# Kernel tuning notes

Measured on AMD Instinct MI355X. Metric: run time of the kernel, lower is better.

The kernel has to match this reference:

```python
import jax, jax.numpy as jnp
import numpy as np

N = 8192        # particles
NBH = 64        # black holes
L = 46.0        # box side -> ~32 neighbors per particle at radius 4.5
K = 4           # kernel_size per axis
KK = K * K * K
EXTENT = 9.0    # radius_scale(1.5) * 6 * particle_radius(1)
EXTENT_BH = 4.0 * EXTENT
EP = 300000     # padded particle-particle edge count
EB = 160000     # padded bh->particle edge count
CIN = 4         # vel(3) + mass(1)
C0, C1, C2, C3 = 32, 64, 64, 3
FOUR_OVER_PI = 4.0 / np.pi


def _ball_query_np(query, points, radius, cap, pad_seg):
    """Brute-force host-side ball query. Returns padded (src, dst); padding
    uses dst == pad_seg (a sentinel segment that is dropped later)."""
    r2 = radius * radius
    src, dst = [], []
    for i in range(0, query.shape[0], 1024):
        q = query[i:i + 1024]
        d2 = ((q[:, None, :] - points[None, :, :]) ** 2).sum(-1)
        m = (d2 < r2) & (d2 > 0.0)  # radius_search_ignore_query_points
        qi, pj = np.nonzero(m)
        dst.append(qi + i)
        src.append(pj)
    src = np.concatenate(src).astype(np.int32)
    dst = np.concatenate(dst).astype(np.int32)
    n = min(len(src), cap)
    out_s = np.zeros(cap, np.int32)
    out_d = np.full(cap, pad_seg, np.int32)
    out_s[:n] = src[:n]
    out_d[:n] = dst[:n]
    return out_s, out_d


def setup_inputs() -> dict:
    rng = np.random.RandomState(0)
    pos = (rng.rand(N, 3) * L).astype(np.float32)
    vel = rng.randn(N, 3).astype(np.float32)
    mass = rng.rand(N).astype(np.float32)
    bh_pos = (rng.rand(NBH, 3) * L).astype(np.float32)
    bh_vel = rng.randn(NBH, 3).astype(np.float32)
    bh_mass = (rng.rand(NBH) * 10.0).astype(np.float32)
    pp_src, pp_dst = _ball_query_np(pos, pos, EXTENT * 0.5, EP, N)
    bh_src, bh_dst = _ball_query_np(pos, bh_pos, EXTENT_BH * 0.5, EB, N)

    def w(*s):
        return (rng.randn(*s) * 0.05).astype(np.float32)

    inp = dict(
        pos=jnp.asarray(pos), vel=jnp.asarray(vel), mass=jnp.asarray(mass),
        bh_pos=jnp.asarray(bh_pos), bh_vel=jnp.asarray(bh_vel), bh_mass=jnp.asarray(bh_mass),
        pp_src=jnp.asarray(pp_src), pp_dst=jnp.asarray(pp_dst),
        bh_src=jnp.asarray(bh_src), bh_dst=jnp.asarray(bh_dst),
        W0a=jnp.asarray(w(K, K, K, CIN, C0)), b0a=jnp.zeros(C0, jnp.float32),
        Wd0=jnp.asarray(w(CIN, C0)), bd0=jnp.zeros(C0, jnp.float32),
        W0b=jnp.asarray(w(K, K, K, CIN, C0)), b0b=jnp.zeros(C0, jnp.float32),
        W1=jnp.asarray(w(K, K, K, 3 * C0, C1)), b1=jnp.zeros(C1, jnp.float32),
        Wd1=jnp.asarray(w(3 * C0, C1)), bd1=jnp.zeros(C1, jnp.float32),
        W2=jnp.asarray(w(K, K, K, C1, C2)), b2=jnp.zeros(C2, jnp.float32),
        Wd2=jnp.asarray(w(C1, C2)), bd2=jnp.zeros(C2, jnp.float32),
        W3=jnp.asarray(w(K, K, K, C2, C3)), b3=jnp.zeros(C3, jnp.float32),
        Wd3=jnp.asarray(w(C2, C3)), bd3=jnp.zeros(C3, jnp.float32),
    )
    return inp


def _ball_to_cube(p):
    """Volume-preserving map from unit ball to cube [-1,1]^3 (sphere->cylinder->cube)."""
    eps = 1e-8
    x, y, z = p[..., 0], p[..., 1], p[..., 2]
    sq = x * x + y * y + z * z
    nrm = jnp.sqrt(sq)
    xy = x * x + y * y
    # sphere -> cylinder
    caps = 1.25 * z * z > xy
    s_caps = jnp.sqrt(3.0 * nrm / (nrm + jnp.abs(z) + eps))
    s_side = nrm / jnp.sqrt(xy + eps)
    s = jnp.where(caps, s_caps, s_side)
    valid = sq > eps
    cx = jnp.where(valid, x * s, 0.0)
    cy = jnp.where(valid, y * s, 0.0)
    cz = jnp.where(valid, jnp.where(caps, jnp.sign(z) * nrm, 1.5 * z), 0.0)
    # cylinder -> cube (concentric disc-to-square, area preserving)
    rxy = jnp.sqrt(cx * cx + cy * cy)
    regA = cx * cx >= cy * cy
    safe_cx = jnp.where(jnp.abs(cx) > eps, cx, 1.0)
    safe_cy = jnp.where(jnp.abs(cy) > eps, cy, 1.0)
    uA = jnp.sign(cx) * rxy
    vA = uA * FOUR_OVER_PI * jnp.arctan(cy / safe_cx)
    vB = jnp.sign(cy) * rxy
    uB = vB * FOUR_OVER_PI * jnp.arctan(cx / safe_cy)
    okxy = rxy > eps
    u = jnp.where(okxy, jnp.where(regA, uA, uB), 0.0)
    v = jnp.where(okxy, jnp.where(regA, vA, vB), 0.0)
    return jnp.stack([u, v, cz], axis=-1)


def _cconv(feats, pos_src, pos_dst, src, dst, W, b, extent):
    """ContinuousConv: ball-query edges (src->dst), poly6 window, trilinear
    kernel interpolation (align_corners=True), scatter-sum, no normalization."""
    n_out = pos_dst.shape[0]
    radius = 0.5 * extent
    ps = jnp.take(pos_src, src, axis=0)                       # [E,3]
    pd = jnp.take(pos_dst, jnp.minimum(dst, n_out - 1), axis=0)
    d = (ps - pd) * (1.0 / radius)                            # normalized offsets
    r_sqr = jnp.sum(d * d, axis=-1)
    win = jnp.clip((1.0 - r_sqr) ** 3, 0.0, 1.0)              # window_poly6
    u = _ball_to_cube(d)                                      # in [-1,1]^3
    t = (u + 1.0) * (0.5 * (K - 1))                           # align_corners grid coords
    i0f = jnp.clip(jnp.floor(t), 0, K - 2)
    i0 = i0f.astype(jnp.int32)
    f = t - i0f                                               # trilinear fractions
    fe = jnp.take(feats, src, axis=0) * win[:, None]          # [E,Cin]
    Cin = feats.shape[1]
    Wf = W.reshape(KK, Cin, -1)
    T = jnp.zeros(((n_out + 1) * KK, Cin), feats.dtype)
    for dx in (0, 1):
        wx = f[:, 0] if dx else 1.0 - f[:, 0]
        for dy in (0, 1):
            wy = f[:, 1] if dy else 1.0 - f[:, 1]
            for dz in (0, 1):
                wz = f[:, 2] if dz else 1.0 - f[:, 2]
                k = ((i0[:, 0] + dx) * K + (i0[:, 1] + dy)) * K + (i0[:, 2] + dz)
                idx = dst * KK + k                            # sentinel dst==n_out dropped
                T = T + jax.ops.segment_sum((wx * wy * wz)[:, None] * fe, idx,
                                            num_segments=(n_out + 1) * KK)
    T = T.reshape(n_out + 1, KK, Cin)[:n_out]                 # [N,64,Cin]
    return jnp.einsum('nkc,kcd->nd', T, Wf) + b


def _forward(pos, vel, mass, bh_pos, bh_vel, bh_mass,
             W0a, b0a, Wd0, bd0, W0b, b0b, W1, b1, Wd1, bd1,
             W2, b2, Wd2, bd2, W3, b3, Wd3, bd3,
             pp_src, pp_dst, bh_src, bh_dst):
    feats = jnp.concatenate([vel, mass[:, None]], axis=-1)        # [N,4]
    bh_feats = jnp.concatenate([bh_vel, bh_mass[:, None]], axis=-1)
    c0 = _cconv(feats, pos, pos, pp_src, pp_dst, W0a, b0a, EXTENT)      # [N,32]
    d0 = feats @ Wd0 + bd0                                               # [N,32]
    cb = _cconv(bh_feats, bh_pos, pos, bh_src, bh_dst, W0b, b0b, EXTENT_BH)
    h = jnp.concatenate([c0, cb, d0], axis=-1)                           # [N,96]
    c1 = jax.nn.relu(_cconv(h, pos, pos, pp_src, pp_dst, W1, b1, EXTENT))
    d1 = jax.nn.relu(h @ Wd1 + bd1)
    h1 = c1 + d1                                                         # 64 != 96 -> no residual
    c2 = jax.nn.relu(_cconv(h1, pos, pos, pp_src, pp_dst, W2, b2, EXTENT))
    d2 = jax.nn.relu(h1 @ Wd2 + bd2)
    h2 = c2 + d2 + h1                                                    # 64 == 64 -> residual
    c3 = _cconv(h2, pos, pos, pp_src, pp_dst, W3, b3, EXTENT)
    d3 = h2 @ Wd3 + bd3
    return c3 + d3                                                       # accelerations [N,3]


def reference(pos, vel, mass, bh_pos, bh_vel, bh_mass,
              pp_src, pp_dst, bh_src, bh_dst,
              W0a, b0a, Wd0, bd0, W0b, b0b, W1, b1, Wd1, bd1,
              W2, b2, Wd2, bd2, W3, b3, Wd3, bd3):
    return _forward(pos, vel, mass, bh_pos, bh_vel, bh_mass,
                    W0a, b0a, Wd0, bd0, W0b, b0b, W1, b1, Wd1, bd1,
                    W2, b2, Wd2, bd2, W3, b3, Wd3, bd3,
                    pp_src, pp_dst, bh_src, bh_dst)
```

## Files before the change

kernel.cpp:

```cpp
#include <hip/hip_runtime.h>
#include <math.h>

#define NPART 8192
#define NBHX  64
#define EPX   300000
#define EBX   160000
#define FOUR_OVER_PI 1.27323954473516f

typedef __attribute__((ext_vector_type(8))) short bf16x8;
typedef __attribute__((ext_vector_type(4))) float f32x4;

__device__ __forceinline__ float signf(float x){ return (x>0.f)?1.f:((x<0.f)?-1.f:0.f); }
__device__ __forceinline__ unsigned short f2bf(float f){
  unsigned u = __float_as_uint(f);
  u += 0x7FFFu + ((u >> 16) & 1u);
  return (unsigned short)(u >> 16);
}
__device__ __forceinline__ float bf2f(unsigned short h){
  return __uint_as_float(((unsigned)h) << 16);
}
__device__ __forceinline__ float bfl(unsigned u){ return __uint_as_float(u << 16); }
__device__ __forceinline__ float bfh(unsigned u){ return __uint_as_float(u & 0xffff0000u); }

__global__ void geom2_kernel(const float* __restrict__ pos, const float* __restrict__ bh_pos,
                             const int* __restrict__ srcP, const int* __restrict__ dstP,
                             const int* __restrict__ srcB, const int* __restrict__ dstB,
                             uint2* __restrict__ gewP, uint2* __restrict__ gewB,
                             int* __restrict__ hist) {
  int idx = blockIdx.x*256 + threadIdx.x;
  if (idx < 4096) hist[idx] = 0;
  bool isP = idx < EPX;
  int e = isP ? idx : idx - EPX;
  if (!isP && e >= EBX) return;
  const int* src = isP ? srcP : srcB;
  const int* dst = isP ? dstP : dstB;
  const float* ppos = isP ? pos : bh_pos;
  uint2* gew = isP ? gewP : gewB;
  float inv_radius = isP ? (1.f/4.5f) : (1.f/18.f);
  int s = src[e], t = dst[e];
  if (t >= NPART) {
    uint2 z; z.x = s*64; z.y = 0;
    for (int j=0;j<8;j++) gew[(size_t)e*8+j] = z;
    return;
  }
  float x = (ppos[s*3+0] - pos[t*3+0]) * inv_radius;
  float y = (ppos[s*3+1] - pos[t*3+1]) * inv_radius;
  float z = (ppos[s*3+2] - pos[t*3+2]) * inv_radius;
  float r2 = x*x + y*y + z*z;
  float w1 = 1.f - r2;
  float win = fminf(fmaxf(w1*w1*w1, 0.f), 1.f);
  const float eps = 1e-8f;
  float nrm = sqrtf(r2);
  float xy = x*x + y*y;
  bool caps = (1.25f*z*z > xy);
  float s_caps = sqrtf(3.f*nrm/(nrm + fabsf(z) + eps));
  float s_side = nrm / sqrtf(xy + eps);
  float sc = caps ? s_caps : s_side;
  bool valid = r2 > eps;
  float cx = valid ? x*sc : 0.f;
  float cy = valid ? y*sc : 0.f;
  float cz = valid ? (caps ? signf(z)*nrm : 1.5f*z) : 0.f;
  float rxy = sqrtf(cx*cx + cy*cy);
  bool regA = (cx*cx >= cy*cy);
  float safe_cx = (fabsf(cx) > eps) ? cx : 1.0f;
  float safe_cy = (fabsf(cy) > eps) ? cy : 1.0f;
  float uA = signf(cx)*rxy;
  float vA = uA * FOUR_OVER_PI * atanf(cy/safe_cx);
  float vB = signf(cy)*rxy;
  float uB = vB * FOUR_OVER_PI * atanf(cx/safe_cy);
  bool okxy = rxy > eps;
  float u = okxy ? (regA ? uA : uB) : 0.f;
  float v = okxy ? (regA ? vA : vB) : 0.f;
  float tt[3] = { (u+1.f)*1.5f, (v+1.f)*1.5f, (cz+1.f)*1.5f };
  int i0[3]; float f[3];
#pragma unroll
  for (int ax=0; ax<3; ax++) {
    float tf = floorf(tt[ax]);
    tf = fminf(fmaxf(tf, 0.f), 2.f);
    i0[ax] = (int)tf;
    f[ax] = tt[ax] - tf;
  }
  unsigned sb = s*64 + ((i0[0]*4 + i0[1])*4 + i0[2]);
#pragma unroll
  for (int j=0;j<8;j++) {
    float wx = (j&4) ? f[0] : 1.f - f[0];
    float wy = (j&2) ? f[1] : 1.f - f[1];
    float wz = (j&1) ? f[2] : 1.f - f[2];
    uint2 o; o.x = sb; o.y = __float_as_uint(win * wx * wy * wz);
    gew[(size_t)e*8+j] = o;
  }
}

__global__ void prep_kernel(const float* __restrict__ vel, const float* __restrict__ mass,
                            const float* __restrict__ bhvel, const float* __restrict__ bhmass,
                            float* __restrict__ feats, float* __restrict__ bhfeats,
                            const int* __restrict__ dstP, const int* __restrict__ dstB,
                            int* __restrict__ rsP, int* __restrict__ rsB) {
  int i = blockIdx.x*256 + threadIdx.x;
  if (i < NPART) {
    feats[i*4+0]=vel[i*3+0]; feats[i*4+1]=vel[i*3+1]; feats[i*4+2]=vel[i*3+2]; feats[i*4+3]=mass[i];
  }
  if (i < NBHX) {
    bhfeats[i*4+0]=bhvel[i*3+0]; bhfeats[i*4+1]=bhvel[i*3+1]; bhfeats[i*4+2]=bhvel[i*3+2]; bhfeats[i*4+3]=bhmass[i];
  }
  if (i <= NPART) {
    int lo = 0, hi = EPX;
    while (lo < hi) { int mid = (lo+hi)>>1; if (dstP[mid] < i) lo = mid+1; else hi = mid; }
    rsP[i] = lo;
  }
  int k = i - (NPART+1);
  if (k >= 0 && k <= NPART) {
    int lo = 0, hi = EBX;
    while (lo < hi) { int mid = (lo+hi)>>1; if (dstB[mid] < k) lo = mid+1; else hi = mid; }
    rsB[k] = lo;
  }
}

__global__ void cellw_kernel(const float* __restrict__ pos, int* __restrict__ cell,
                             int* __restrict__ hist,
                             const float* __restrict__ W1, const float* __restrict__ W2,
                             const float* __restrict__ W3,
                             unsigned short* __restrict__ BT1, unsigned short* __restrict__ BT2,
                             unsigned short* __restrict__ BT3) {
  int b = blockIdx.x;
  if (b < 32) {
    int i = b*256 + threadIdx.x;
    const float inv = 16.0f/46.0f;
    int ix = min(15, max(0, (int)(pos[i*3+0]*inv)));
    int iy = min(15, max(0, (int)(pos[i*3+1]*inv)));
    int iz = min(15, max(0, (int)(pos[i*3+2]*inv)));
    int c = (ix*16+iy)*16+iz;
    cell[i] = c;
    atomicAdd(&hist[c], 1);
    return;
  }
  int idx = (b-32)*256 + threadIdx.x;
  const int S1 = 4096*96, S2 = 4096*64, S3 = 256*64;
  if (idx < S1) {
    int n = idx/96, c = idx - n*96; int k = n>>6, d = n&63;
    BT1[idx] = f2bf(W1[((size_t)k*96 + c)*64 + d]);
  } else if (idx < S1+S2) {
    int t = idx - S1; int n = t>>6, c = t&63; int k = n>>6, d = n&63;
    BT2[t] = f2bf(W2[((size_t)k*64 + c)*64 + d]);
  } else if (idx < S1+S2+S3) {
    int t = idx - S1 - S2; int n = t>>6, c = t&63; int k = n>>2, d = n&3;
    BT3[t] = f2bf((d < 3) ? W3[((size_t)k*64 + c)*3 + d] : 0.f);
  }
}

__global__ __launch_bounds__(256) void scan_kernel(const int* __restrict__ hist, int* __restrict__ offs) {
  __shared__ int wsum[4];
  int t = threadIdx.x;
  int base = t*16;
  int loc[16]; int s = 0;
#pragma unroll
  for (int i=0;i<16;i++){ loc[i]=s; s+=hist[base+i]; }
  int lane = t & 63, wv = t >> 6;
  int pre = s;
  for (int off=1; off<64; off<<=1) {
    int v = __shfl_up(pre, off);
    if (lane >= off) pre += v;
  }
  if (lane == 63) wsum[wv] = pre;
  __syncthreads();
  int wbase = 0;
  for (int w=0; w<wv; w++) wbase += wsum[w];
  int ex = wbase + pre - s;
#pragma unroll
  for (int i=0;i<16;i++) offs[base+i] = ex + loc[i];
}
__global__ void scatterorder_kernel(const int* __restrict__ cell, int* __restrict__ offs,
                                    int* __restrict__ order) {
  int i = blockIdx.x*256 + threadIdx.x;
  if (i >= NPART) return;
  int p = atomicAdd(&offs[cell[i]], 1);
  order[p] = i;
}

__device__ __forceinline__ int swz_block(int bid, int nb) {
  return (bid & 7)*(nb >> 3) + (bid >> 3);
}

__global__ void y0_kernel(const float* __restrict__ feats4, const float* __restrict__ bhfeats,
                          const float* __restrict__ W0a, const float* __restrict__ W0b,
                          unsigned short* __restrict__ Y0a, unsigned short* __restrict__ Y0b) {
  int idx = blockIdx.x*256 + threadIdx.x;
  if (idx >= (NPART+NBHX)*256) return;
  int oct = idx & 3, k = (idx>>2) & 63, s = idx >> 8;
  bool bh = (s >= NPART);
  int sl = bh ? s - NPART : s;
  const float* fp = (bh ? bhfeats : feats4) + (size_t)sl*4;
  const float* W0 = bh ? W0b : W0a;
  unsigned short* Y = (bh ? Y0b : Y0a) + ((size_t)sl*64 + k)*32 + oct*8;
  float4 f = *(const float4*)fp;
  const float* w = W0 + (size_t)k*128 + oct*8;
  unsigned short o[8];
#pragma unroll
  for (int i=0;i<8;i++) {
    float v = f.x*w[i] + f.y*w[32+i] + f.z*w[64+i] + f.w*w[96+i];
    o[i] = f2bf(v);
  }
  uint4 u;
  u.x = (unsigned)o[0] | ((unsigned)o[1]<<16);
  u.y = (unsigned)o[2] | ((unsigned)o[3]<<16);
  u.z = (unsigned)o[4] | ((unsigned)o[5]<<16);
  u.w = (unsigned)o[6] | ((unsigned)o[7]<<16);
  *(uint4*)Y = u;
}

__global__ __launch_bounds__(256) void gemm_y_kernel(
    const unsigned short* __restrict__ A, const unsigned short* __restrict__ BT,
    int KC, int Ntot, unsigned short* __restrict__ Y) {
  const int wid  = threadIdx.x >> 6;
  const int lane = threadIdx.x & 63;
// ... 16 lines not shown
      bf16x8 b = *(const bf16x8*)(BT + (size_t)(n0 + n*16 + r)*KC + ko);
      acc[0][n] = __builtin_amdgcn_mfma_f32_16x16x32_bf16(a0, b, acc[0][n], 0, 0, 0);
      acc[1][n] = __builtin_amdgcn_mfma_f32_16x16x32_bf16(a1, b, acc[1][n], 0, 0, 0);
    }
  }
#pragma unroll
  for (int h=0;h<2;h++)
#pragma unroll
    for (int n=0;n<4;n++)
#pragma unroll
      for (int j=0;j<4;j++)
        Y[(size_t)(m0 + h*16 + g*4 + j)*Ntot + n0 + n*16 + r] = f2bf(acc[h][n][j]);
}

__device__ __forceinline__ void xor_add4(f32x4& a, int mask) {
  a.x += __shfl_xor(a.x, mask);
  a.y += __shfl_xor(a.y, mask);
  a.z += __shfl_xor(a.z, mask);
  a.w += __shfl_xor(a.w, mask);
}

__global__ __launch_bounds__(256) void gather_l0_kernel(
    const int* __restrict__ order,
    const int* __restrict__ rsP, const uint2* __restrict__ gewP,
    const int* __restrict__ rsB, const uint2* __restrict__ gewB,
    const unsigned short* __restrict__ Y0a, const unsigned short* __restrict__ Y0b,
    const float* __restrict__ feats4, const float* __restrict__ Wd0, const float* __restrict__ bd0,
    const float* __restrict__ b0a, const float* __restrict__ b0b,
    float* __restrict__ hf, unsigned short* __restrict__ hb) {
  const int sw = swz_block(blockIdx.x, gridDim.x);
  const int node = order[sw*4 + (threadIdx.x >> 6)];
  const int lane = threadIdx.x & 63;
  const int j = lane >> 3, cg = lane & 7;
  const int koff = ((j&4)<<2) | ((j&2)<<1) | (j&1);
  f32x4 accP = {0.f,0.f,0.f,0.f}, accB = {0.f,0.f,0.f,0.f};
  {
    int e0 = rsP[node], e1 = rsP[node+1];
    int e = e0;
    for (; e + 4 <= e1; e += 4) {
      uint2 p[4]; uint2 y[4];
#pragma unroll
      for (int i=0;i<4;i++) p[i] = gewP[(size_t)(e+i)*8 + j];
#pragma unroll
      for (int i=0;i<4;i++) y[i] = *(const uint2*)(Y0a + ((size_t)(p[i].x + koff))*32 + cg*4);
#pragma unroll
      for (int i=0;i<4;i++) {
        float w = __uint_as_float(p[i].y);
        accP.x += w*bfl(y[i].x); accP.y += w*bfh(y[i].x);
        accP.z += w*bfl(y[i].y); accP.w += w*bfh(y[i].y);
      }
    }
    for (; e < e1; e++) {
      uint2 p = gewP[(size_t)e*8 + j];
      uint2 y = *(const uint2*)(Y0a + ((size_t)(p.x + koff))*32 + cg*4);
      float w = __uint_as_float(p.y);
      accP.x += w*bfl(y.x); accP.y += w*bfh(y.x);
      accP.z += w*bfl(y.y); accP.w += w*bfh(y.y);
    }
  }
  {
    int e0 = rsB[node], e1 = rsB[node+1];
    int e = e0;
    for (; e + 4 <= e1; e += 4) {
      uint2 p[4]; uint2 y[4];
#pragma unroll
      for (int i=0;i<4;i++) p[i] = gewB[(size_t)(e+i)*8 + j];
#pragma unroll
      for (int i=0;i<4;i++) y[i] = *(const uint2*)(Y0b + ((size_t)(p[i].x + koff))*32 + cg*4);
#pragma unroll
      for (int i=0;i<4;i++) {
        float w = __uint_as_float(p[i].y);
        accB.x += w*bfl(y[i].x); accB.y += w*bfh(y[i].x);
        accB.z += w*bfl(y[i].y); accB.w += w*bfh(y[i].y);
      }
    }
    for (; e < e1; e++) {
      uint2 p = gewB[(size_t)e*8 + j];
      uint2 y = *(const uint2*)(Y0b + ((size_t)(p.x + koff))*32 + cg*4);
      float w = __uint_as_float(p.y);
      accB.x += w*bfl(y.x); accB.y += w*bfh(y.x);
      accB.z += w*bfl(y.y); accB.w += w*bfh(y.y);
    }
  }
  xor_add4(accP, 8);  xor_add4(accP, 16); xor_add4(accP, 32);
  xor_add4(accB, 8);  xor_add4(accB, 16); xor_add4(accB, 32);
  if (lane < 8) {
    float4 f = *(const float4*)(feats4 + (size_t)node*4);
    float4 ba = *(const float4*)(b0a + cg*4);
    float4 bb = *(const float4*)(b0b + cg*4);
    float4 bdv = *(const float4*)(bd0 + cg*4);
    float4 w0v = *(const float4*)(Wd0 + 0*32 + cg*4);
    float4 w1v = *(const float4*)(Wd0 + 1*32 + cg*4);
    float4 w2v = *(const float4*)(Wd0 + 2*32 + cg*4);
    float4 w3v = *(const float4*)(Wd0 + 3*32 + cg*4);
    float4 dd;
    dd.x = bdv.x + f.x*w0v.x + f.y*w1v.x + f.z*w2v.x + f.w*w3v.x;
    dd.y = bdv.y + f.x*w0v.y + f.y*w1v.y + f.z*w2v.y + f.w*w3v.y;
    dd.z = bdv.z + f.x*w0v.z + f.y*w1v.z + f.z*w2v.z + f.w*w3v.z;
    dd.w = bdv.w + f.x*w0v.w + f.y*w1v.w + f.z*w2v.w + f.w*w3v.w;
    float4 c0; c0.x = accP.x + ba.x; c0.y = accP.y + ba.y; c0.z = accP.z + ba.z; c0.w = accP.w + ba.w;
    float4 cb; cb.x = accB.x + bb.x; cb.y = accB.y + bb.y; cb.z = accB.z + bb.z; cb.w = accB.w + bb.w;
    size_t o = (size_t)node*96;
    *(float4*)(hf + o + cg*4)      = c0;
    *(float4*)(hf + o + 32 + cg*4) = cb;
    *(float4*)(hf + o + 64 + cg*4) = dd;
    ushort4 u0 = {f2bf(c0.x), f2bf(c0.y), f2bf(c0.z), f2bf(c0.w)};
    ushort4 u1 = {f2bf(cb.x), f2bf(cb.y), f2bf(cb.z), f2bf(cb.w)};
    ushort4 u2 = {f2bf(dd.x), f2bf(dd.y), f2bf(dd.z), f2bf(dd.w)};
    *(ushort4*)(hb + o + cg*4)      = u0;
    *(ushort4*)(hb + o + 32 + cg*4) = u1;
    *(ushort4*)(hb + o + 64 + cg*4) = u2;
  }
}

template<int DCIN, bool ADDSKIP>
__global__ __launch_bounds__(128) void gather64_kernel(
    const int* __restrict__ order,
    const int* __restrict__ rs, const uint2* __restrict__ gew,
    const unsigned short* __restrict__ Y,
    const float* __restrict__ Xf, const float* __restrict__ Wd, const float* __restrict__ bd,
    const float* __restrict__ bconv, const float* __restrict__ skip,
    float* __restrict__ outf, unsigned short* __restrict__ outb) {
  const int sw = swz_block(blockIdx.x, gridDim.x);
  const int node = order[sw];
  const int wave = threadIdx.x >> 6;
  const int lane = threadIdx.x & 63;
  const int j = lane >> 3, cg = lane & 7;
  const int koff = ((j&4)<<2) | ((j&2)<<1) | (j&1);
  __shared__ __align__(16) float red[64*16];
  f32x4 accA = {0.f,0.f,0.f,0.f}, accB = {0.f,0.f,0.f,0.f};
  const int e0 = rs[node], e1 = rs[node+1];
  int e = e0 + wave;
  for (; e + 6 < e1; e += 8) {
    uint2 p[4]; uint4 y[4];
#pragma unroll
    for (int i=0;i<4;i++) p[i] = gew[(size_t)(e + i*2)*8 + j];
#pragma unroll
    for (int i=0;i<4;i++) y[i] = *(const uint4*)(Y + ((size_t)(p[i].x + koff))*64 + cg*8);
#pragma unroll
    for (int i=0;i<4;i++) {
      float w = __uint_as_float(p[i].y);
      accA.x += w*bfl(y[i].x); accA.y += w*bfh(y[i].x);
      accA.z += w*bfl(y[i].y); accA.w += w*bfh(y[i].y);
      accB.x += w*bfl(y[i].z); accB.y += w*bfh(y[i].z);
      accB.z += w*bfl(y[i].w); accB.w += w*bfh(y[i].w);
    }
  }
  for (; e < e1; e += 2) {
    uint2 p = gew[(size_t)e*8 + j];
    uint4 y = *(const uint4*)(Y + ((size_t)(p.x + koff))*64 + cg*8);
    float w = __uint_as_float(p.y);
    accA.x += w*bfl(y.x); accA.y += w*bfh(y.x);
    accA.z += w*bfl(y.y); accA.w += w*bfh(y.y);
    accB.x += w*bfl(y.z); accB.y += w*bfh(y.z);
    accB.z += w*bfl(y.w); accB.w += w*bfh(y.w);
  }
  constexpr int KQ = DCIN/16;
  f32x4 ddA = {0.f,0.f,0.f,0.f}, ddB = {0.f,0.f,0.f,0.f};
  {
    const int seg = wave*8 + j;
    const float* x = Xf + (size_t)node*DCIN + seg*KQ;
#pragma unroll
    for (int kk=0; kk<KQ; kk++) {
      float xv = x[kk];
      float4 w0 = *(const float4*)(Wd + (size_t)(seg*KQ+kk)*64 + cg*8);
      float4 w1 = *(const float4*)(Wd + (size_t)(seg*KQ+kk)*64 + cg*8 + 4);
      ddA.x += xv*w0.x; ddA.y += xv*w0.y; ddA.z += xv*w0.z; ddA.w += xv*w0.w;
      ddB.x += xv*w1.x; ddB.y += xv*w1.y; ddB.z += xv*w1.z; ddB.w += xv*w1.w;
    }
  }
  if (wave == 1) {
    *(f32x4*)(red + lane*16)      = accA;
    *(f32x4*)(red + lane*16 + 4)  = accB;
    *(f32x4*)(red + lane*16 + 8)  = ddA;
    *(f32x4*)(red + lane*16 + 12) = ddB;
  }
  __syncthreads();
  if (wave == 0) {
    {
      f32x4 oA = *(const f32x4*)(red + lane*16);
      f32x4 oB = *(const f32x4*)(red + lane*16 + 4);
      f32x4 oC = *(const f32x4*)(red + lane*16 + 8);
      f32x4 oD = *(const f32x4*)(red + lane*16 + 12);
      accA.x += oA.x; accA.y += oA.y; accA.z += oA.z; accA.w += oA.w;
      accB.x += oB.x; accB.y += oB.y; accB.z += oB.z; accB.w += oB.w;
      ddA.x += oC.x; ddA.y += oC.y; ddA.z += oC.z; ddA.w += oC.w;
      ddB.x += oD.x; ddB.y += oD.y; ddB.z += oD.z; ddB.w += oD.w;
    }
    xor_add4(accA, 8); xor_add4(accA, 16); xor_add4(accA, 32);
    xor_add4(accB, 8); xor_add4(accB, 16); xor_add4(accB, 32);
    xor_add4(ddA, 8);  xor_add4(ddA, 16);  xor_add4(ddA, 32);
    xor_add4(ddB, 8);  xor_add4(ddB, 16);  xor_add4(ddB, 32);
    if (lane < 8) {
      float4 bc0 = *(const float4*)(bconv + cg*8);
      float4 bc1 = *(const float4*)(bconv + cg*8 + 4);
      float4 bd0v = *(const float4*)(bd + cg*8);
      float4 bd1v = *(const float4*)(bd + cg*8 + 4);
      float4 v0, v1;
      v0.x = fmaxf(accA.x + bc0.x, 0.f) + fmaxf(ddA.x + bd0v.x, 0.f);
      v0.y = fmaxf(accA.y + bc0.y, 0.f) + fmaxf(ddA.y + bd0v.y, 0.f);
      v0.z = fmaxf(accA.z + bc0.z, 0.f) + fmaxf(ddA.z + bd0v.z, 0.f);
      v0.w = fmaxf(accA.w + bc0.w, 0.f) + fmaxf(ddA.w + bd0v.w, 0.f);
      v1.x = fmaxf(accB.x + bc1.x, 0.f) + fmaxf(ddB.x + bd1v.x, 0.f);
      v1.y = fmaxf(accB.y + bc1.y, 0.f) + fmaxf(ddB.y + bd1v.y, 0.f);
      v1.z = fmaxf(accB.z + bc1.z, 0.f) + fmaxf(ddB.z + bd1v.z, 0.f);
      v1.w = fmaxf(accB.w + bc1.w, 0.f) + fmaxf(ddB.w + bd1v.w, 0.f);
      if (ADDSKIP) {
        float4 s0 = *(const float4*)(skip + (size_t)node*64 + cg*8);
        float4 s1 = *(const float4*)(skip + (size_t)node*64 + cg*8 + 4);
        v0.x += s0.x; v0.y += s0.y; v0.z += s0.z; v0.w += s0.w;
        v1.x += s1.x; v1.y += s1.y; v1.z += s1.z; v1.w += s1.w;
      }
      *(float4*)(outf + (size_t)node*64 + cg*8)     = v0;
      *(float4*)(outf + (size_t)node*64 + cg*8 + 4) = v1;
      ushort4 u0 = {f2bf(v0.x), f2bf(v0.y), f2bf(v0.z), f2bf(v0.w)};
      ushort4 u1 = {f2bf(v1.x), f2bf(v1.y), f2bf(v1.z), f2bf(v1.w)};
      *(ushort4*)(outb + (size_t)node*64 + cg*8)     = u0;
      *(ushort4*)(outb + (size_t)node*64 + cg*8 + 4) = u1;
    }
  }
}

__global__ __launch_bounds__(256) void gather3_kernel(
    const int* __restrict__ order,
    const int* __restrict__ rs, const uint2* __restrict__ gew,
    const unsigned short* __restrict__ Y3,
    const float* __restrict__ h2f, const float* __restrict__ Wd3, const float* __restrict__ bd3,
    const float* __restrict__ b3, float* __restrict__ out) {
  const int sw = swz_block(blockIdx.x, gridDim.x);
  const int node = order[sw*4 + (threadIdx.x >> 6)];
  const int lane = threadIdx.x & 63;
  const int e2 = lane >> 5, j = (lane >> 2) & 7, dd = lane & 3;
  const int koff = ((j&4)<<2)|((j&2)<<1)|(j&1);
  float acc = 0.f;
  const int e0 = rs[node], e1 = rs[node+1];
  for (int e = e0; e < e1; e += 2) {
    int ee = e + e2;
    bool v = ee < e1;
    int ix = v ? ee : e;
    uint2 p = gew[(size_t)ix*8 + j];
    float w = v ? __uint_as_float(p.y) : 0.f;
    acc += w * bf2f(Y3[((size_t)(p.x + koff))*4 + dd]);
  }
  acc += __shfl_xor(acc, 4);
  acc += __shfl_xor(acc, 8);
  acc += __shfl_xor(acc, 16);
  acc += __shfl_down(acc, 32);
  if (lane < 3) {
    float d3 = bd3[lane];
    const float* x = h2f + (size_t)node*64;
#pragma unroll 8
    for (int c=0;c<64;c++) d3 += x[c]*Wd3[c*3 + lane];
    out[(size_t)node*3 + lane] = acc + b3[lane] + d3;
  }
}

extern "C" void kernel_launch(void* const* d_in, const int* in_sizes, int n_in,
                              void* d_out, int out_size, void* d_ws, size_t ws_size,
                              hipStream_t stream) {
  const float* pos    = (const float*)d_in[0];
  const float* vel    = (const float*)d_in[1];
  const float* mass   = (const float*)d_in[2];
  const float* bh_pos = (const float*)d_in[3];
  const float* bh_vel = (const float*)d_in[4];
  const float* bh_mass= (const float*)d_in[5];
  const int* pp_src   = (const int*)d_in[6];
  const int* pp_dst   = (const int*)d_in[7];
  const int* bh_src   = (const int*)d_in[8];
  const int* bh_dst   = (const int*)d_in[9];
  const float* W0a=(const float*)d_in[10]; const float* b0a=(const float*)d_in[11];
  const float* Wd0=(const float*)d_in[12]; const float* bd0=(const float*)d_in[13];
  const float* W0b=(const float*)d_in[14]; const float* b0b=(const float*)d_in[15];
  const float* W1 =(const float*)d_in[16]; const float* b1 =(const float*)d_in[17];
  const float* Wd1=(const float*)d_in[18]; const float* bd1=(const float*)d_in[19];
  const float* W2 =(const float*)d_in[20]; const float* b2 =(const float*)d_in[21];
  const float* Wd2=(const float*)d_in[22]; const float* bd2=(const float*)d_in[23];
  const float* W3 =(const float*)d_in[24]; const float* b3 =(const float*)d_in[25];
  const float* Wd3=(const float*)d_in[26]; const float* bd3=(const float*)d_in[27];
  float* out = (float*)d_out;
  char* wsb = (char*)d_ws;

  size_t off = 0;
  auto alloc = [&](size_t nbytes){ size_t o = off; off += (nbytes + 255) & ~((size_t)255); return o; };
  size_t feats_o   = alloc((size_t)NPART*4*4);
  size_t bhfeats_o = alloc((size_t)NBHX*4*4);
  size_t rs_pp_o   = alloc(8256*4);
  size_t rs_bh_o   = alloc(8256*4);
  size_t gew_pp_o  = alloc((size_t)EPX*8*8);
  size_t gew_bh_o  = alloc((size_t)EBX*8*8);
  size_t hf_o  = alloc((size_t)NPART*96*4);
  size_t hb_o  = alloc((size_t)NPART*96*2);
  size_t h1f_o = alloc((size_t)NPART*64*4);
  size_t h1b_o = alloc((size_t)NPART*64*2);
  size_t h2f_o = alloc((size_t)NPART*64*4);
  size_t h2b_o = alloc((size_t)NPART*64*2);
  size_t bt1_o = alloc((size_t)4096*96*2);
  size_t bt2_o = alloc((size_t)4096*64*2);
  size_t bt3_o = alloc((size_t)256*64*2);
  size_t y0b_o = alloc((size_t)NBHX*64*32*2);
  size_t cell_o = alloc((size_t)NPART*4);
  size_t hist_o = alloc((size_t)4096*4);
  size_t order_o= alloc((size_t)NPART*4);
  size_t y_o   = alloc((size_t)NPART*4096*2);

  float* featsP = (float*)(wsb + feats_o); float* bhfeatsP = (float*)(wsb + bhfeats_o);
  int* rsPP = (int*)(wsb + rs_pp_o); int* rsBH = (int*)(wsb + rs_bh_o);
  uint2* gewP = (uint2*)(wsb + gew_pp_o);
  uint2* gewB = (uint2*)(wsb + gew_bh_o);
  float* hf  = (float*)(wsb + hf_o);  unsigned short* hb  = (unsigned short*)(wsb + hb_o);
  float* h1f = (float*)(wsb + h1f_o); unsigned short* h1b = (unsigned short*)(wsb + h1b_o);
  float* h2f = (float*)(wsb + h2f_o); unsigned short* h2b = (unsigned short*)(wsb + h2b_o);
  unsigned short* BT1 = (unsigned short*)(wsb + bt1_o);
  unsigned short* BT2 = (unsigned short*)(wsb + bt2_o);
  unsigned short* BT3 = (unsigned short*)(wsb + bt3_o);
  unsigned short* Y0b = (unsigned short*)(wsb + y0b_o);
  int* cellA = (int*)(wsb + cell_o);
  int* histA = (int*)(wsb + hist_o);
  int* orderA= (int*)(wsb + order_o);
  unsigned short* Ybuf = (unsigned short*)(wsb + y_o);

  geom2_kernel<<<(EPX+EBX+255)/256, 256, 0, stream>>>(pos, bh_pos, pp_src, pp_dst, bh_src, bh_dst,
                                                      gewP, gewB, histA);
  prep_kernel<<<(2*(NPART+1)+255)/256, 256, 0, stream>>>(vel, mass, bh_vel, bh_mass,
                                                         featsP, bhfeatsP, pp_dst, bh_dst, rsPP, rsBH);
  cellw_kernel<<<32 + (4096*96 + 4096*64 + 256*64 + 255)/256, 256, 0, stream>>>(
      pos, cellA, histA, W1, W2, W3, BT1, BT2, BT3);
  scan_kernel<<<1, 256, 0, stream>>>(histA, histA);
  scatterorder_kernel<<<NPART/256, 256, 0, stream>>>(cellA, histA, orderA);

  y0_kernel<<<((NPART+NBHX)*256+255)/256, 256, 0, stream>>>(featsP, bhfeatsP, W0a, W0b, Ybuf, Y0b);
  gather_l0_kernel<<<NPART/4, 256, 0, stream>>>(orderA, rsPP, gewP, rsBH, gewB,
                                                Ybuf, Y0b, featsP, Wd0, bd0, b0a, b0b, hf, hb);
  {
    dim3 g(NPART/128, 4096/64);
    gemm_y_kernel<<<g, 256, 0, stream>>>(hb, BT1, 96, 4096, Ybuf);
    gather64_kernel<96,false><<<NPART, 128, 0, stream>>>(orderA, rsPP, gewP, Ybuf,
        hf, Wd1, bd1, b1, nullptr, h1f, h1b);
  }
  {
    dim3 g(NPART/128, 4096/64);
    gemm_y_kernel<<<g, 256, 0, stream>>>(h1b, BT2, 64, 4096, Ybuf);
    gather64_kernel<64,true><<<NPART, 128, 0, stream>>>(orderA, rsPP, gewP, Ybuf,
        h1f, Wd2, bd2, b2, h1f, h2f, h2b);
  }
  {
    dim3 g(NPART/128, 256/64);
    gemm_y_kernel<<<g, 256, 0, stream>>>(h2b, BT3, 64, 256, Ybuf);
    gather3_kernel<<<NPART/4, 256, 0, stream>>>(orderA, rsPP, gewP, Ybuf,
        h2f, Wd3, bd3, b3, out);
  }
}
```

Before: 219.6 us.

## Compress edge records to one 16-byte entry and store features in spatial order

Each edge used to be written as 8 corner entries of index plus weight. It is now a single 16-byte record: a base index, fp16 fractional coordinates and two z-weights pre-multiplied by the window. The gather kernels rebuild each corner weight on the fly, which cuts edge-table traffic in every layer pass. Intermediate features (Y, hf, h1, h2) are now stored in the spatially sorted order through an inverse permutation, so gathered rows are more likely to be local in cache. The costs are a few extra multiplies per gathered corner, fp16 rounding of the fractions, and a reordering of kernel launches so geometry runs after the sort.

```diff
diff --git a/kernel.cpp b/kernel.cpp
--- a/kernel.cpp
+++ b/kernel.cpp
@@ -21,26 +21,135 @@
 }
 __device__ __forceinline__ float bfl(unsigned u){ return __uint_as_float(u << 16); }
 __device__ __forceinline__ float bfh(unsigned u){ return __uint_as_float(u & 0xffff0000u); }
+__device__ __forceinline__ float f16tof(unsigned short h){
+  _Float16 v = __builtin_bit_cast(_Float16, h);
+  return (float)v;
+}
+__device__ __forceinline__ unsigned short ftof16(float f){
+  _Float16 v = (_Float16)f;
+  return __builtin_bit_cast(unsigned short, v);
+}
+__device__ __forceinline__ float corner_w(const uint4& r, int j){
+  float fx = f16tof((unsigned short)(r.y & 0xffffu));
+  float fy = f16tof((unsigned short)(r.y >> 16));
+  float wx = (j&4) ? fx : 1.f - fx;
+  float wy = (j&2) ? fy : 1.f - fy;
+  float wz = __uint_as_float((j&1) ? r.w : r.z);
+  return wx*wy*wz;
+}
+
+__global__ void prep_kernel(const float* __restrict__ vel, const float* __restrict__ mass,
+                            const float* __restrict__ bhvel, const float* __restrict__ bhmass,
+                            float* __restrict__ feats, float* __restrict__ bhfeats,
+                            const int* __restrict__ dstP, const int* __restrict__ dstB,
+                            int* __restrict__ rsP, int* __restrict__ rsB,
+                            int* __restrict__ hist) {
+  int i = blockIdx.x*256 + threadIdx.x;
+  if (i < 4096) hist[i] = 0;
+  if (i < NPART) {
+    feats[i*4+0]=vel[i*3+0]; feats[i*4+1]=vel[i*3+1]; feats[i*4+2]=vel[i*3+2]; feats[i*4+3]=mass[i];
+  }
+  if (i < NBHX) {
+    bhfeats[i*4+0]=bhvel[i*3+0]; bhfeats[i*4+1]=bhvel[i*3+1]; bhfeats[i*4+2]=bhvel[i*3+2]; bhfeats[i*4+3]=bhmass[i];
+  }
+  if (i <= NPART) {
+    int lo = 0, hi = EPX;
+    while (lo < hi) { int mid = (lo+hi)>>1; if (dstP[mid] < i) lo = mid+1; else hi = mid; }
+    rsP[i] = lo;
+  }
+  int k = i - (NPART+1);
+  if (k >= 0 && k <= NPART) {
+    int lo = 0, hi = EBX;
+    while (lo < hi) { int mid = (lo+hi)>>1; if (dstB[mid] < k) lo = mid+1; else hi = mid; }
+    rsB[k] = lo;
+  }
+}
+
+__global__ void cellw_kernel(const float* __restrict__ pos, int* __restrict__ cell,
+                             int* __restrict__ hist,
+                             const float* __restrict__ W1, const float* __restrict__ W2,
+                             const float* __restrict__ W3,
+                             unsigned short* __restrict__ BT1, unsigned short* __restrict__ BT2,
+                             unsigned short* __restrict__ BT3) {
+  int b = blockIdx.x;
+  if (b < 32) {
+    int i = b*256 + threadIdx.x;
+    const float inv = 16.0f/46.0f;
+    int ix = min(15, max(0, (int)(pos[i*3+0]*inv)));
+    int iy = min(15, max(0, (int)(pos[i*3+1]*inv)));
+    int iz = min(15, max(0, (int)(pos[i*3+2]*inv)));
+    int c = (ix*16+iy)*16+iz;
+    cell[i] = c;
+    atomicAdd(&hist[c], 1);
+    return;
+  }
+  int idx = (b-32)*256 + threadIdx.x;
+  const int S1 = 4096*96, S2 = 4096*64, S3 = 256*64;
+  if (idx < S1) {
+    int n = idx/96, c = idx - n*96; int k = n>>6, d = n&63;
+    BT1[idx] = f2bf(W1[((size_t)k*96 + c)*64 + d]);
+  } else if (idx < S1+S2) {
+    int t = idx - S1; int n = t>>6, c = t&63; int k = n>>6, d = n&63;
+    BT2[t] = f2bf(W2[((size_t)k*64 + c)*64 + d]);
+  } else if (idx < S1+S2+S3) {
+    int t = idx - S1 - S2; int n = t>>6, c = t&63; int k = n>>2, d = n&3;
+    BT3[t] = f2bf((d < 3) ? W3[((size_t)k*64 + c)*3 + d] : 0.f);
+  }
+}
+
+__global__ __launch_bounds__(256) void scan_kernel(const int* __restrict__ hist, int* __restrict__ offs) {
+  __shared__ int wsum[4];
+  int t = threadIdx.x;
+  int base = t*16;
+  int loc[16]; int s = 0;
+#pragma unroll
+  for (int i=0;i<16;i++){ loc[i]=s; s+=hist[base+i]; }
+  int lane = t & 63, wv = t >> 6;
+  int pre = s;
+  for (int off=1; off<64; off<<=1) {
+    int v = __shfl_up(pre, off);
+    if (lane >= off) pre += v;
+  }
+  if (lane == 63) wsum[wv] = pre;
+  __syncthreads();
+  int wbase = 0;
+  for (int w=0; w<wv; w++) wbase += wsum[w];
+  int ex = wbase + pre - s;
+#pragma unroll
+  for (int i=0;i<16;i++) offs[base+i] = ex + loc[i];
+}
+__global__ void scatterorder_kernel(const int* __restrict__ cell, int* __restrict__ offs,
+                                    int* __restrict__ order, int* __restrict__ invp) {
+  int i = blockIdx.x*256 + threadIdx.x;
+  if (i >= NPART) return;
+  int p = atomicAdd(&offs[cell[i]], 1);
+  order[p] = i;
+  invp[i] = p;
+}
+
+__device__ __forceinline__ int swz_block(int bid, int nb) {
+  return (bid & 7)*(nb >> 3) + (bid >> 3);
+}
 
 __global__ void geom2_kernel(const float* __restrict__ pos, const float* __restrict__ bh_pos,
                              const int* __restrict__ srcP, const int* __restrict__ dstP,
                              const int* __restrict__ srcB, const int* __restrict__ dstB,
-                             uint2* __restrict__ gewP, uint2* __restrict__ gewB,
-                             int* __restrict__ hist) {
+                             const int* __restrict__ invp,
+                             uint4* __restrict__ recP, uint4* __restrict__ recB) {
   int idx = blockIdx.x*256 + threadIdx.x;
-  if (idx < 4096) hist[idx] = 0;
   bool isP = idx < EPX;
   int e = isP ? idx : idx - EPX;
   if (!isP && e >= EBX) return;
   const int* src = isP ? srcP : srcB;
   const int* dst = isP ? dstP : dstB;
   const float* ppos = isP ? pos : bh_pos;
-  uint2* gew = isP ? gewP : gewB;
+  uint4* rec = isP ? recP : recB;
   float inv_radius = isP ? (1.f/4.5f) : (1.f/18.f);
   int s = src[e], t = dst[e];
+  unsigned srow = isP ? (unsigned)invp[s] : (unsigned)s;
   if (t >= NPART) {
-    uint2 z; z.x = s*64; z.y = 0;
-    for (int j=0;j<8;j++) gew[(size_t)e*8+j] = z;
+    uint4 z; z.x = srow*64; z.y = 0; z.z = 0; z.w = 0;
+    rec[e] = z;
     return;
   }
   float x = (ppos[s*3+0] - pos[t*3+0]) * inv_radius;
@@ -80,108 +189,16 @@
     i0[ax] = (int)tf;
     f[ax] = tt[ax] - tf;
   }
-  unsigned sb = s*64 + ((i0[0]*4 + i0[1])*4 + i0[2]);
-#pragma unroll
-  for (int j=0;j<8;j++) {
-    float wx = (j&4) ? f[0] : 1.f - f[0];
-    float wy = (j&2) ? f[1] : 1.f - f[1];
-    float wz = (j&1) ? f[2] : 1.f - f[2];
-    uint2 o; o.x = sb; o.y = __float_as_uint(win * wx * wy * wz);
-    gew[(size_t)e*8+j] = o;
-  }
-}
-
-__global__ void prep_kernel(const float* __restrict__ vel, const float* __restrict__ mass,
-                            const float* __restrict__ bhvel, const float* __restrict__ bhmass,
-                            float* __restrict__ feats, float* __restrict__ bhfeats,
-                            const int* __restrict__ dstP, const int* __restrict__ dstB,
-                            int* __restrict__ rsP, int* __restrict__ rsB) {
-  int i = blockIdx.x*256 + threadIdx.x;
-  if (i < NPART) {
-    feats[i*4+0]=vel[i*3+0]; feats[i*4+1]=vel[i*3+1]; feats[i*4+2]=vel[i*3+2]; feats[i*4+3]=mass[i];
-  }
-  if (i < NBHX) {
-    bhfeats[i*4+0]=bhvel[i*3+0]; bhfeats[i*4+1]=bhvel[i*3+1]; bhfeats[i*4+2]=bhvel[i*3+2]; bhfeats[i*4+3]=bhmass[i];
-  }
-  if (i <= NPART) {
-    int lo = 0, hi = EPX;
-    while (lo < hi) { int mid = (lo+hi)>>1; if (dstP[mid] < i) lo = mid+1; else hi = mid; }
-    rsP[i] = lo;
-  }
-  int k = i - (NPART+1);
-  if (k >= 0 && k <= NPART) {
-    int lo = 0, hi = EBX;
-    while (lo < hi) { int mid = (lo+hi)>>1; if (dstB[mid] < k) lo = mid+1; else hi = mid; }
-    rsB[k] = lo;
-  }
-}
-
-__global__ void cellw_kernel(const float* __restrict__ pos, int* __restrict__ cell,
-                             int* __restrict__ hist,
-                             const float* __restrict__ W1, const float* __restrict__ W2,
-                             const float* __restrict__ W3,
-                             unsigned short* __restrict__ BT1, unsigned short* __restrict__ BT2,
-                             unsigned short* __restrict__ BT3) {
-  int b = blockIdx.x;
-  if (b < 32) {
-    int i = b*256 + threadIdx.x;
-    const float inv = 16.0f/46.0f;
-    int ix = min(15, max(0, (int)(pos[i*3+0]*inv)));
-    int iy = min(15, max(0, (int)(pos[i*3+1]*inv)));
-    int iz = min(15, max(0, (int)(pos[i*3+2]*inv)));
-    int c = (ix*16+iy)*16+iz;
-    cell[i] = c;
-    atomicAdd(&hist[c], 1);
-    return;
-  }
-  int idx = (b-32)*256 + threadIdx.x;
-  const int S1 = 4096*96, S2 = 4096*64, S3 = 256*64;
-  if (idx < S1) {
-    int n = idx/96, c = idx - n*96; int k = n>>6, d = n&63;
-    BT1[idx] = f2bf(W1[((size_t)k*96 + c)*64 + d]);
-  } else if (idx < S1+S2) {
-    int t = idx - S1; int n = t>>6, c = t&63; int k = n>>6, d = n&63;
-    BT2[t] = f2bf(W2[((size_t)k*64 + c)*64 + d]);
-  } else if (idx < S1+S2+S3) {
-    int t = idx - S1 - S2; int n = t>>6, c = t&63; int k = n>>2, d = n&3;
-    BT3[t] = f2bf((d < 3) ? W3[((size_t)k*64 + c)*3 + d] : 0.f);
-  }
-}
-
-__global__ __launch_bounds__(256) void scan_kernel(const int* __restrict__ hist, int* __restrict__ offs) {
-  __shared__ int wsum[4];
-  int t = threadIdx.x;
-  int base = t*16;
-  int loc[16]; int s = 0;
-#pragma unroll
-  for (int i=0;i<16;i++){ loc[i]=s; s+=hist[base+i]; }
-  int lane = t & 63, wv = t >> 6;
-  int pre = s;
-  for (int off=1; off<64; off<<=1) {
-    int v = __shfl_up(pre, off);
-    if (lane >= off) pre += v;
-  }
-  if (lane == 63) wsum[wv] = pre;
-  __syncthreads();
-  int wbase = 0;
-  for (int w=0; w<wv; w++) wbase += wsum[w];
-  int ex = wbase + pre - s;
-#pragma unroll
-  for (int i=0;i<16;i++) offs[base+i] = ex + loc[i];
-}
-__global__ void scatterorder_kernel(const int* __restrict__ cell, int* __restrict__ offs,
-                                    int* __restrict__ order) {
-  int i = blockIdx.x*256 + threadIdx.x;
-  if (i >= NPART) return;
-  int p = atomicAdd(&offs[cell[i]], 1);
-  order[p] = i;
-}
-
-__device__ __forceinline__ int swz_block(int bid, int nb) {
-  return (bid & 7)*(nb >> 3) + (bid >> 3);
-}
-
-__global__ void y0_kernel(const float* __restrict__ feats4, const float* __restrict__ bhfeats,
+  uint4 o;
+  o.x = srow*64 + ((i0[0]*4 + i0[1])*4 + i0[2]);
+  o.y = (unsigned)ftof16(f[0]) | ((unsigned)ftof16(f[1]) << 16);
+  o.z = __float_as_uint(win * (1.f - f[2]));
+  o.w = __float_as_uint(win * f[2]);
+  rec[e] = o;
+}
+
+__global__ void y0_kernel(const int* __restrict__ order,
+                          const float* __restrict__ feats4, const float* __restrict__ bhfeats,
                           const float* __restrict__ W0a, const float* __restrict__ W0b,
                           unsigned short* __restrict__ Y0a, unsigned short* __restrict__ Y0b) {
   int idx = blockIdx.x*256 + threadIdx.x;
@@ -189,7 +206,8 @@
   int oct = idx & 3, k = (idx>>2) & 63, s = idx >> 8;
   bool bh = (s >= NPART);
   int sl = bh ? s - NPART : s;
-  const float* fp = (bh ? bhfeats : feats4) + (size_t)sl*4;
+  int srcn = bh ? sl : order[sl];
+  const float* fp = (bh ? bhfeats : feats4) + (size_t)srcn*4;
   const float* W0 = bh ? W0b : W0a;
   unsigned short* Y = (bh ? Y0b : Y0a) + ((size_t)sl*64 + k)*32 + oct*8;
   float4 f = *(const float4*)fp;
@@ -252,14 +270,15 @@
 
 __global__ __launch_bounds__(256) void gather_l0_kernel(
     const int* __restrict__ order,
-    const int* __restrict__ rsP, const uint2* __restrict__ gewP,
-    const int* __restrict__ rsB, const uint2* __restrict__ gewB,
+    const int* __restrict__ rsP, const uint4* __restrict__ recP,
+    const int* __restrict__ rsB, const uint4* __restrict__ recB,
     const unsigned short* __restrict__ Y0a, const unsigned short* __restrict__ Y0b,
     const float* __restrict__ feats4, const float* __restrict__ Wd0, const float* __restrict__ bd0,
     const float* __restrict__ b0a, const float* __restrict__ b0b,
     float* __restrict__ hf, unsigned short* __restrict__ hb) {
   const int sw = swz_block(blockIdx.x, gridDim.x);
-  const int node = order[sw*4 + (threadIdx.x >> 6)];
+  const int p4 = sw*4 + (threadIdx.x >> 6);
+  const int node = order[p4];
   const int lane = threadIdx.x & 63;
   const int j = lane >> 3, cg = lane & 7;
   const int koff = ((j&4)<<2) | ((j&2)<<1) | (j&1);
@@ -268,22 +287,22 @@
     int e0 = rsP[node], e1 = rsP[node+1];
     int e = e0;
     for (; e + 4 <= e1; e += 4) {
-      uint2 p[4]; uint2 y[4];
-#pragma unroll
-      for (int i=0;i<4;i++) p[i] = gewP[(size_t)(e+i)*8 + j];
-#pragma unroll
-      for (int i=0;i<4;i++) y[i] = *(const uint2*)(Y0a + ((size_t)(p[i].x + koff))*32 + cg*4);
+      uint4 r[4]; uint2 y[4];
+#pragma unroll
+      for (int i=0;i<4;i++) r[i] = recP[e+i];
+#pragma unroll
+      for (int i=0;i<4;i++) y[i] = *(const uint2*)(Y0a + ((size_t)(r[i].x + koff))*32 + cg*4);
 #pragma unroll
       for (int i=0;i<4;i++) {
-        float w = __uint_as_float(p[i].y);
+        float w = corner_w(r[i], j);
         accP.x += w*bfl(y[i].x); accP.y += w*bfh(y[i].x);
         accP.z += w*bfl(y[i].y); accP.w += w*bfh(y[i].y);
       }
     }
     for (; e < e1; e++) {
-      uint2 p = gewP[(size_t)e*8 + j];
-      uint2 y = *(const uint2*)(Y0a + ((size_t)(p.x + koff))*32 + cg*4);
-      float w = __uint_as_float(p.y);
+      uint4 r = recP[e];
+      uint2 y = *(const uint2*)(Y0a + ((size_t)(r.x + koff))*32 + cg*4);
+      float w = corner_w(r, j);
       accP.x += w*bfl(y.x); accP.y += w*bfh(y.x);
       accP.z += w*bfl(y.y); accP.w += w*bfh(y.y);
     }
@@ -292,22 +311,22 @@
     int e0 = rsB[node], e1 = rsB[node+1];
     int e = e0;
     for (; e + 4 <= e1; e += 4) {
-      uint2 p[4]; uint2 y[4];
-#pragma unroll
-      for (int i=0;i<4;i++) p[i] = gewB[(size_t)(e+i)*8 + j];
-#pragma unroll
-      for (int i=0;i<4;i++) y[i] = *(const uint2*)(Y0b + ((size_t)(p[i].x + koff))*32 + cg*4);
+      uint4 r[4]; uint2 y[4];
+#pragma unroll
+      for (int i=0;i<4;i++) r[i] = recB[e+i];
+#pragma unroll
+      for (int i=0;i<4;i++) y[i] = *(const uint2*)(Y0b + ((size_t)(r[i].x + koff))*32 + cg*4);
 #pragma unroll
       for (int i=0;i<4;i++) {
-        float w = __uint_as_float(p[i].y);
+        float w = corner_w(r[i], j);
         accB.x += w*bfl(y[i].x); accB.y += w*bfh(y[i].x);
         accB.z += w*bfl(y[i].y); accB.w += w*bfh(y[i].y);
       }
     }
     for (; e < e1; e++) {
-      uint2 p = gewB[(size_t)e*8 + j];
-      uint2 y = *(const uint2*)(Y0b + ((size_t)(p.x + koff))*32 + cg*4);
-      float w = __uint_as_float(p.y);
+      uint4 r = recB[e];
+      uint2 y = *(const uint2*)(Y0b + ((size_t)(r.x + koff))*32 + cg*4);
+      float w = corner_w(r, j);
       accB.x += w*bfl(y.x); accB.y += w*bfh(y.x);
       accB.z += w*bfl(y.y); accB.w += w*bfh(y.y);
     }
@@ -330,7 +349,7 @@
     dd.w = bdv.w + f.x*w0v.w + f.y*w1v.w + f.z*w2v.w + f.w*w3v.w;
     float4 c0; c0.x = accP.x + ba.x; c0.y = accP.y + ba.y; c0.z = accP.z + ba.z; c0.w = accP.w + ba.w;
     float4 cb; cb.x = accB.x + bb.x; cb.y = accB.y + bb.y; cb.z = accB.z + bb.z; cb.w = accB.w + bb.w;
-    size_t o = (size_t)node*96;
+    size_t o = (size_t)p4*96;
     *(float4*)(hf + o + cg*4)      = c0;
     *(float4*)(hf + o + 32 + cg*4) = cb;
     *(float4*)(hf + o + 64 + cg*4) = dd;
@@ -346,13 +365,13 @@
 template<int DCIN, bool ADDSKIP>
 __global__ __launch_bounds__(128) void gather64_kernel(
     const int* __restrict__ order,
-    const int* __restrict__ rs, const uint2* __restrict__ gew,
+    const int* __restrict__ rs, const uint4* __restrict__ rec,
     const unsigned short* __restrict__ Y,
     const float* __restrict__ Xf, const float* __restrict__ Wd, const float* __restrict__ bd,
     const float* __restrict__ bconv, const float* __restrict__ skip,
     float* __restrict__ outf, unsigned short* __restrict__ outb) {
-  const int sw = swz_block(blockIdx.x, gridDim.x);
-  const int node = order[sw];
+  const int p = swz_block(blockIdx.x, gridDim.x);
+  const int node = order[p];
   const int wave = threadIdx.x >> 6;
   const int lane = threadIdx.x & 63;
   const int j = lane >> 3, cg = lane & 7;
@@ -362,14 +381,14 @@
   const int e0 = rs[node], e1 = rs[node+1];
   int e = e0 + wave;
   for (; e + 6 < e1; e += 8) {
-    uint2 p[4]; uint4 y[4];
-#pragma unroll
-    for (int i=0;i<4;i++) p[i] = gew[(size_t)(e + i*2)*8 + j];
-#pragma unroll
-    for (int i=0;i<4;i++) y[i] = *(const uint4*)(Y + ((size_t)(p[i].x + koff))*64 + cg*8);
+    uint4 r[4]; uint4 y[4];
+#pragma unroll
+    for (int i=0;i<4;i++) r[i] = rec[e + i*2];
+#pragma unroll
+    for (int i=0;i<4;i++) y[i] = *(const uint4*)(Y + ((size_t)(r[i].x + koff))*64 + cg*8);
 #pragma unroll
     for (int i=0;i<4;i++) {
-      float w = __uint_as_float(p[i].y);
+      float w = corner_w(r[i], j);
       accA.x += w*bfl(y[i].x); accA.y += w*bfh(y[i].x);
       accA.z += w*bfl(y[i].y); accA.w += w*bfh(y[i].y);
       accB.x += w*bfl(y[i].z); accB.y += w*bfh(y[i].z);
@@ -377,9 +396,9 @@
     }
   }
   for (; e < e1; e += 2) {
-    uint2 p = gew[(size_t)e*8 + j];
-    uint4 y = *(const uint4*)(Y + ((size_t)(p.x + koff))*64 + cg*8);
-    float w = __uint_as_float(p.y);
+    uint4 r = rec[e];
+    uint4 y = *(const uint4*)(Y + ((size_t)(r.x + koff))*64 + cg*8);
+    float w = corner_w(r, j);
     accA.x += w*bfl(y.x); accA.y += w*bfh(y.x);
     accA.z += w*bfl(y.y); accA.w += w*bfh(y.y);
     accB.x += w*bfl(y.z); accB.y += w*bfh(y.z);
@@ -389,7 +408,7 @@
   f32x4 ddA = {0.f,0.f,0.f,0.f}, ddB = {0.f,0.f,0.f,0.f};
   {
     const int seg = wave*8 + j;
-    const float* x = Xf + (size_t)node*DCIN + seg*KQ;
+    const float* x = Xf + (size_t)p*DCIN + seg*KQ;
 #pragma unroll
     for (int kk=0; kk<KQ; kk++) {
       float xv = x[kk];
@@ -436,29 +455,30 @@
       v1.z = fmaxf(accB.z + bc1.z, 0.f) + fmaxf(ddB.z + bd1v.z, 0.f);
       v1.w = fmaxf(accB.w + bc1.w, 0.f) + fmaxf(ddB.w + bd1v.w, 0.f);
       if (ADDSKIP) {
-        float4 s0 = *(const float4*)(skip + (size_t)node*64 + cg*8);
-        float4 s1 = *(const float4*)(skip + (size_t)node*64 + cg*8 + 4);
+        float4 s0 = *(const float4*)(skip + (size_t)p*64 + cg*8);
+        float4 s1 = *(const float4*)(skip + (size_t)p*64 + cg*8 + 4);
         v0.x += s0.x; v0.y += s0.y; v0.z += s0.z; v0.w += s0.w;
         v1.x += s1.x; v1.y += s1.y; v1.z += s1.z; v1.w += s1.w;
       }
-      *(float4*)(outf + (size_t)node*64 + cg*8)     = v0;
-      *(float4*)(outf + (size_t)node*64 + cg*8 + 4) = v1;
+      *(float4*)(outf + (size_t)p*64 + cg*8)     = v0;
+      *(float4*)(outf + (size_t)p*64 + cg*8 + 4) = v1;
       ushort4 u0 = {f2bf(v0.x), f2bf(v0.y), f2bf(v0.z), f2bf(v0.w)};
       ushort4 u1 = {f2bf(v1.x), f2bf(v1.y), f2bf(v1.z), f2bf(v1.w)};
-      *(ushort4*)(outb + (size_t)node*64 + cg*8)     = u0;
-      *(ushort4*)(outb + (size_t)node*64 + cg*8 + 4) = u1;
+      *(ushort4*)(outb + (size_t)p*64 + cg*8)     = u0;
+      *(ushort4*)(outb + (size_t)p*64 + cg*8 + 4) = u1;
     }
   }
 }
 
 __global__ __launch_bounds__(256) void gather3_kernel(
     const int* __restrict__ order,
-    const int* __restrict__ rs, const uint2* __restrict__ gew,
+    const int* __restrict__ rs, const uint4* __restrict__ rec,
     const unsigned short* __restrict__ Y3,
     const float* __restrict__ h2f, const float* __restrict__ Wd3, const float* __restrict__ bd3,
     const float* __restrict__ b3, float* __restrict__ out) {
   const int sw = swz_block(blockIdx.x, gridDim.x);
-  const int node = order[sw*4 + (threadIdx.x >> 6)];
+  const int p4 = sw*4 + (threadIdx.x >> 6);
+  const int node = order[p4];
   const int lane = threadIdx.x & 63;
   const int e2 = lane >> 5, j = (lane >> 2) & 7, dd = lane & 3;
   const int koff = ((j&4)<<2)|((j&2)<<1)|(j&1);
@@ -468,9 +488,9 @@
     int ee = e + e2;
     bool v = ee < e1;
     int ix = v ? ee : e;
-    uint2 p = gew[(size_t)ix*8 + j];
-    float w = v ? __uint_as_float(p.y) : 0.f;
-    acc += w * bf2f(Y3[((size_t)(p.x + koff))*4 + dd]);
+    uint4 r = rec[ix];
+    float w = v ? corner_w(r, j) : 0.f;
+    acc += w * bf2f(Y3[((size_t)(r.x + koff))*4 + dd]);
   }
   acc += __shfl_xor(acc, 4);
   acc += __shfl_xor(acc, 8);
@@ -478,7 +498,7 @@
   acc += __shfl_down(acc, 32);
   if (lane < 3) {
     float d3 = bd3[lane];
-    const float* x = h2f + (size_t)node*64;
+    const float* x = h2f + (size_t)p4*64;
 #pragma unroll 8
     for (int c=0;c<64;c++) d3 += x[c]*Wd3[c*3 + lane];
     out[(size_t)node*3 + lane] = acc + b3[lane] + d3;
@@ -516,8 +536,8 @@
   size_t bhfeats_o = alloc((size_t)NBHX*4*4);
   size_t rs_pp_o   = alloc(8256*4);
   size_t rs_bh_o   = alloc(8256*4);
-  size_t gew_pp_o  = alloc((size_t)EPX*8*8);
-  size_t gew_bh_o  = alloc((size_t)EBX*8*8);
+  size_t rec_pp_o  = alloc((size_t)EPX*16);
+  size_t rec_bh_o  = alloc((size_t)EBX*16);
   size_t hf_o  = alloc((size_t)NPART*96*4);
   size_t hb_o  = alloc((size_t)NPART*96*2);
   size_t h1f_o = alloc((size_t)NPART*64*4);
@@ -531,12 +551,13 @@
   size_t cell_o = alloc((size_t)NPART*4);
   size_t hist_o = alloc((size_t)4096*4);
   size_t order_o= alloc((size_t)NPART*4);
+  size_t inv_o  = alloc((size_t)NPART*4);
   size_t y_o   = alloc((size_t)NPART*4096*2);
 
   float* featsP = (float*)(wsb + feats_o); float* bhfeatsP = (float*)(wsb + bhfeats_o);
   int* rsPP = (int*)(wsb + rs_pp_o); int* rsBH = (int*)(wsb + rs_bh_o);
-  uint2* gewP = (uint2*)(wsb + gew_pp_o);
-  uint2* gewB = (uint2*)(wsb + gew_bh_o);
+  uint4* recP = (uint4*)(wsb + rec_pp_o);
+  uint4* recB = (uint4*)(wsb + rec_bh_o);
   float* hf  = (float*)(wsb + hf_o);  unsigned short* hb  = (unsigned short*)(wsb + hb_o);
   float* h1f = (float*)(wsb + h1f_o); unsigned short* h1b = (unsigned short*)(wsb + h1b_o);
   float* h2f = (float*)(wsb + h2f_o); unsigned short* h2b = (unsigned short*)(wsb + h2b_o);
@@ -547,36 +568,38 @@
   int* cellA = (int*)(wsb + cell_o);
   int* histA = (int*)(wsb + hist_o);
   int* orderA= (int*)(wsb + order_o);
+  int* invA  = (int*)(wsb + inv_o);
   unsigned short* Ybuf = (unsigned short*)(wsb + y_o);
 
-  geom2_kernel<<<(EPX+EBX+255)/256, 256, 0, stream>>>(pos, bh_pos, pp_src, pp_dst, bh_src, bh_dst,
-                                                      gewP, gewB, histA);
   prep_kernel<<<(2*(NPART+1)+255)/256, 256, 0, stream>>>(vel, mass, bh_vel, bh_mass,
-                                                         featsP, bhfeatsP, pp_dst, bh_dst, rsPP, rsBH);
+                                                         featsP, bhfeatsP, pp_dst, bh_dst,
+                                                         rsPP, rsBH, histA);
   cellw_kernel<<<32 + (4096*96 + 4096*64 + 256*64 + 255)/256, 256, 0, stream>>>(
       pos, cellA, histA, W1, W2, W3, BT1, BT2, BT3);
   scan_kernel<<<1, 256, 0, stream>>>(histA, histA);
-  scatterorder_kernel<<<NPART/256, 256, 0, stream>>>(cellA, histA, orderA);
-
-  y0_kernel<<<((NPART+NBHX)*256+255)/256, 256, 0, stream>>>(featsP, bhfeatsP, W0a, W0b, Ybuf, Y0b);
-  gather_l0_kernel<<<NPART/4, 256, 0, stream>>>(orderA, rsPP, gewP, rsBH, gewB,
+  scatterorder_kernel<<<NPART/256, 256, 0, stream>>>(cellA, histA, orderA, invA);
+  geom2_kernel<<<(EPX+EBX+255)/256, 256, 0, stream>>>(pos, bh_pos, pp_src, pp_dst, bh_src, bh_dst,
+                                                      invA, recP, recB);
+
+  y0_kernel<<<((NPART+NBHX)*256+255)/256, 256, 0, stream>>>(orderA, featsP, bhfeatsP, W0a, W0b, Ybuf, Y0b);
+  gather_l0_kernel<<<NPART/4, 256, 0, stream>>>(orderA, rsPP, recP, rsBH, recB,
                                                 Ybuf, Y0b, featsP, Wd0, bd0, b0a, b0b, hf, hb);
   {
     dim3 g(NPART/128, 4096/64);
     gemm_y_kernel<<<g, 256, 0, stream>>>(hb, BT1, 96, 4096, Ybuf);
-    gather64_kernel<96,false><<<NPART, 128, 0, stream>>>(orderA, rsPP, gewP, Ybuf,
+    gather64_kernel<96,false><<<NPART, 128, 0, stream>>>(orderA, rsPP, recP, Ybuf,
         hf, Wd1, bd1, b1, nullptr, h1f, h1b);
   }
   {
     dim3 g(NPART/128, 4096/64);
     gemm_y_kernel<<<g, 256, 0, stream>>>(h1b, BT2, 64, 4096, Ybuf);
-    gather64_kernel<64,true><<<NPART, 128, 0, stream>>>(orderA, rsPP, gewP, Ybuf,
+    gather64_kernel<64,true><<<NPART, 128, 0, stream>>>(orderA, rsPP, recP, Ybuf,
         h1f, Wd2, bd2, b2, h1f, h2f, h2b);
   }
   {
     dim3 g(NPART/128, 256/64);
     gemm_y_kernel<<<g, 256, 0, stream>>>(h2b, BT3, 64, 256, Ybuf);
-    gather3_kernel<<<NPART/4, 256, 0, stream>>>(orderA, rsPP, gewP, Ybuf,
+    gather3_kernel<<<NPART/4, 256, 0, stream>>>(orderA, rsPP, recP, Ybuf,
         h2f, Wd3, bd3, b3, out);
   }
 }
```

After: 211.3 us. 1.04x faster.
